# Kernel tuning notes

Hardware: AMD Instinct MI355X
Metric: run time of the kernel (lower is better)

Reference implementation:

```python
import jax, jax.numpy as jnp
import numpy as np

B, N, C = 2, 2048, 1024
H = 16
D = C // H  # head_dim = 64
SCALE = D ** -0.5


def setup_inputs() -> dict:
    key = jax.random.key(0)
    k1, k2, k3, k4 = jax.random.split(key, 4)
    x = jax.random.normal(k1, (B, N, C), dtype=jnp.float32)
    # nn.Linear(in_dim, 3*out_dim, bias=False): store as [in, 3*out] for x @ W
    w_qkv = jax.random.normal(k2, (C, 3 * C), dtype=jnp.float32) * (C ** -0.5)
    w_proj = jax.random.normal(k3, (C, C), dtype=jnp.float32) * (C ** -0.5)
    b_proj = jax.random.normal(k4, (C,), dtype=jnp.float32) * 0.01
    return {"x": x, "w_qkv": w_qkv, "w_proj": w_proj, "b_proj": b_proj}


def reference(x, w_qkv, w_proj, b_proj):
    b, n, c = x.shape
    # QKV projection -> [3, B, H, N, D]
    qkv = (x @ w_qkv).reshape(b, n, 3, H, D).transpose(2, 0, 3, 1, 4)
    q, k, v = qkv[0], qkv[1], qkv[2]
    # scaled dot-product attention, full [B, H, N, N] scores as in original
    attn = jax.nn.softmax(jnp.einsum('bhqd,bhkd->bhqk', q * SCALE, k), axis=-1)
    out = jnp.einsum('bhqk,bhkd->bhqd', attn, v)  # [B, H, N, D]
    out = out.transpose(0, 2, 1, 3).reshape(b, n, c)
    return out @ w_proj + b_proj
```

## Files before the change

### kernel.cpp

```cpp
#include <hip/hip_runtime.h>

typedef unsigned short u16;
typedef float f32x4 __attribute__((ext_vector_type(4)));
typedef short bf16x8 __attribute__((ext_vector_type(8)));
typedef u16 u16x4 __attribute__((ext_vector_type(4)));
typedef u16 u16x8 __attribute__((ext_vector_type(8)));
typedef __bf16 bfr4 __attribute__((ext_vector_type(4)));

#define BB 2
#define NN 2048
#define CC 1024
#define HH 16
#define DD 64
#define MM (BB * NN)
#define NQKV (3 * CC)
#define QSCALE 0.18033688011112042f

#if __has_builtin(__builtin_amdgcn_exp2f)
#define EXP2(x) __builtin_amdgcn_exp2f(x)
#else
#define EXP2(x) exp2f(x)
#endif

__device__ __forceinline__ u16 f2bf(float f) {
    unsigned u = __float_as_uint(f);
    u += 0x7FFFu + ((u >> 16) & 1u);
    return (u16)(u >> 16);
}

__device__ __forceinline__ void ld_lds16(const u16* g, u16* l) {
    __builtin_amdgcn_global_load_lds(
        (const __attribute__((address_space(1))) unsigned int*)g,
        (__attribute__((address_space(3))) unsigned int*)l, 16, 0, 0);
}

__global__ __launch_bounds__(256) void k_prep(const float* __restrict__ x,
                                              const float* __restrict__ wqkv,
                                              const float* __restrict__ wproj,
                                              u16* __restrict__ Xb,
                                              u16* __restrict__ Wq,
                                              u16* __restrict__ Wp) {
    __shared__ float tile[64][65];
    int bid = blockIdx.x, t = threadIdx.x;
    if (bid < 2048) {
        int i = (bid * 256 + t) * 8;
        float4 a = *(const float4*)(x + i);
        float4 b = *(const float4*)(x + i + 4);
        u16x8 o;
        o[0] = f2bf(a.x); o[1] = f2bf(a.y); o[2] = f2bf(a.z); o[3] = f2bf(a.w);
        o[4] = f2bf(b.x); o[5] = f2bf(b.y); o[6] = f2bf(b.z); o[7] = f2bf(b.w);
        *(u16x8*)(Xb + i) = o;
        return;
    }
    const float* in;
    u16* out;
    int Nn, n0, k0;
    if (bid < 2048 + 768) {
        int b2 = bid - 2048;
        in = wqkv; out = Wq; Nn = NQKV;
        n0 = (b2 % 48) * 64; k0 = (b2 / 48) * 64;
    } else {
        int b3 = bid - 2816;
        in = wproj; out = Wp; Nn = CC;
        n0 = (b3 & 15) * 64; k0 = (b3 >> 4) * 64;
    }
    int tx = t & 63, ty = t >> 6;
#pragma unroll
    for (int r = 0; r < 64; r += 4)
        tile[ty + r][tx] = in[(size_t)(k0 + ty + r) * Nn + n0 + tx];
    __syncthreads();
#pragma unroll
    for (int r = 0; r < 64; r += 4)
        out[(size_t)(n0 + ty + r) * CC + k0 + tx] = f2bf(tile[tx][ty + r]);
}

__global__ __launch_bounds__(512, 2) void k_gemmq(
    const u16* __restrict__ A, const u16* __restrict__ B,
    u16* __restrict__ Qb, u16* __restrict__ Kb, u16* __restrict__ Vb) {
    const int Kd = 1024;
    __shared__ __align__(16) u16 Ah0[256][64], Bh0[192][64];
    __shared__ __align__(16) u16 Ah1[256][64], Bh1[192][64];

    int t = threadIdx.x, wave = t >> 6, lane = t & 63;
    int quad = lane >> 4, l16 = lane & 15;
    int wr = wave >> 2, wc = wave & 3;

    int cid = blockIdx.y * 16 + blockIdx.x;
    int swz = (cid & 7) * 32 + (cid >> 3);
    int m0 = (swz >> 4) * 256, n0 = (swz & 15) * 192;

    int strow = wave * 8 + (lane >> 3);
    int stdst = (lane & 7) * 8;
    int stsrc = ((lane & 7) ^ (lane >> 3)) * 8;

    f32x4 acc[8][3];
#pragma unroll
    for (int i = 0; i < 8; i++)
#pragma unroll
        for (int j = 0; j < 3; j++) acc[i][j] = f32x4{0.f, 0.f, 0.f, 0.f};

    auto STAGE = [&](int k0, u16 (*Ad)[64], u16 (*Bd)[64]) {
#pragma unroll
        for (int i = 0; i < 4; i++) {
            int row = i * 64 + strow;
            ld_lds16(A + (size_t)(m0 + row) * Kd + k0 + stsrc, &Ad[row][stdst]);
        }
#pragma unroll
        for (int i = 0; i < 3; i++) {
            int row = i * 64 + strow;
            ld_lds16(B + (size_t)(n0 + row) * Kd + k0 + stsrc, &Bd[row][stdst]);
        }
    };
    auto COMPUTE = [&](u16 (*As)[64], u16 (*Bs)[64]) {
#pragma unroll
        for (int s = 0; s < 2; s++) {
            int pos = ((s * 4 + quad) ^ (l16 & 7)) * 8;
            bf16x8 af[8], bg[3];
#pragma unroll
            for (int m = 0; m < 8; m++)
                af[m] = *(const bf16x8*)&As[wr * 128 + m * 16 + l16][pos];
#pragma unroll
            for (int n = 0; n < 3; n++)
                bg[n] = *(const bf16x8*)&Bs[wc * 48 + n * 16 + l16][pos];
            __builtin_amdgcn_s_setprio(1);
#pragma unroll
            for (int m = 0; m < 8; m++)
#pragma unroll
                for (int n = 0; n < 3; n++)
                    acc[m][n] = __builtin_amdgcn_mfma_f32_16x16x32_bf16(
                        af[m], bg[n], acc[m][n], 0, 0, 0);
            __builtin_amdgcn_s_setprio(0);
        }
    };

    STAGE(0, Ah0, Bh0);
    __syncthreads();
    for (int k0 = 0; k0 < Kd; k0 += 128) {
        STAGE(k0 + 64, Ah1, Bh1);
        COMPUTE(Ah0, Bh0);
        __syncthreads();
        if (k0 + 128 < Kd) STAGE(k0 + 128, Ah0, Bh0);
        COMPUTE(Ah1, Bh1);
        __syncthreads();
    }

#pragma unroll
    for (int m = 0; m < 8; m++)
#pragma unroll
        for (int n = 0; n < 3; n++)
#pragma unroll
            for (int r = 0; r < 4; r++) {
                int grow = m0 + wr * 128 + m * 16 + quad * 4 + r;
                int gcol = n0 + wc * 48 + n * 16 + l16;
                float v = acc[m][n][r];
                int three = gcol >> 10, rem = gcol & 1023;
                int h = rem >> 6, d = rem & 63;
                int bb = grow >> 11, nn = grow & 2047;
                if (three == 0) {
                    Qb[((size_t)(bb * HH + h) * NN + nn) * DD + d] = f2bf(v * QSCALE);
                } else if (three == 1) {
                    Kb[((size_t)(bb * HH + h) * NN + nn) * DD + d] = f2bf(v);
                } else {
                    Vb[((size_t)(bb * HH + h) * DD + d) * NN + nn] = f2bf(v);
                }
            }
}

__global__ __launch_bounds__(256) void k_gemmp(
    const u16* __restrict__ A, const u16* __restrict__ B,
    const float* __restrict__ bias, float* __restrict__ Cout) {
    const int Kd = 1024;
    __shared__ __align__(16) u16 Ah[64][128];
    __shared__ __align__(16) u16 Bh[128][128];

    int t = threadIdx.x, wave = t >> 6, lane = t & 63;
    int quad = lane >> 4, l16 = lane & 15;
    int m0 = blockIdx.x * 64, n0 = blockIdx.y * 128;

    int strow = lane >> 4;
    int stdst = (lane & 15) * 8;

    f32x4 acc[4][2];
#pragma unroll
    for (int i = 0; i < 4; i++)
#pragma unroll
        for (int j = 0; j < 2; j++) acc[i][j] = f32x4{0.f, 0.f, 0.f, 0.f};

    auto STAGE = [&](int k0) {
#pragma unroll
        for (int i = 0; i < 4; i++) {
            int row = wave * 16 + i * 4 + strow;
            int src = ((lane & 15) ^ (row & 7)) * 8;
            ld_lds16(A + (size_t)(m0 + row) * Kd + k0 + src, &Ah[row & 63][0] + stdst);
        }
#pragma unroll
        for (int i = 0; i < 8; i++) {
            int row = wave * 32 + i * 4 + strow;
            int src = ((lane & 15) ^ (row & 7)) * 8;
            ld_lds16(B + (size_t)(n0 + row) * Kd + k0 + src, &Bh[row & 127][0] + stdst);
        }
    };
    auto COMPUTE = [&]() {
#pragma unroll
        for (int s = 0; s < 4; s++) {
            int pos = ((s * 4 + quad) ^ (l16 & 7)) * 8;
            bf16x8 af[4], bg[2];
#pragma unroll
            for (int m = 0; m < 4; m++)
                af[m] = *(const bf16x8*)&Ah[m * 16 + l16][pos];
#pragma unroll
            for (int n = 0; n < 2; n++)
                bg[n] = *(const bf16x8*)&Bh[wave * 32 + n * 16 + l16][pos];
            __builtin_amdgcn_s_setprio(1);
#pragma unroll
            for (int m = 0; m < 4; m++)
#pragma unroll
                for (int n = 0; n < 2; n++)
                    acc[m][n] = __builtin_amdgcn_mfma_f32_16x16x32_bf16(
                        af[m], bg[n], acc[m][n], 0, 0, 0);
            __builtin_amdgcn_s_setprio(0);
        }
    };

    for (int k0 = 0; k0 < Kd; k0 += 128) {
        __syncthreads();
        STAGE(k0);
        __syncthreads();
        COMPUTE();
    }

#pragma unroll
    for (int m = 0; m < 4; m++)
#pragma unroll
        for (int n = 0; n < 2; n++)
#pragma unroll
            for (int r = 0; r < 4; r++) {
                int grow = m0 + m * 16 + quad * 4 + r;
                int gcol = n0 + wave * 32 + n * 16 + l16;
                Cout[(size_t)grow * CC + gcol] = acc[m][n][r] + bias[gcol];
            }
}

__global__ __launch_bounds__(512) void k_attn(const u16* __restrict__ Qb,
                                              const u16* __restrict__ Kb,
                                              const u16* __restrict__ VbT,
                                              u16* __restrict__ Ob) {
    __shared__ __align__(16) u16 Ks0[64][64], Ks1[64][64];
    __shared__ __align__(16) u16 Vs0[64][64], Vs1[64][64];
    __shared__ __align__(16) u16 Ps[8][32][72];

    int t = threadIdx.x, wave = t >> 6, lane = t & 63;
    int quad = lane >> 4, l16 = lane & 15;
    int bh = blockIdx.x, q0 = blockIdx.y * 256;
    const size_t kbase = (size_t)bh * NN * DD;
    const size_t vbase = (size_t)bh * DD * NN;

    bf16x8 qf[2][2];
#pragma unroll
    for (int qj = 0; qj < 2; qj++) {
        int qrow = q0 + wave * 32 + qj * 16 + l16;
        qf[qj][0] = *(const bf16x8*)&Qb[kbase + (size_t)qrow * DD + quad * 8];
        qf[qj][1] = *(const bf16x8*)&Qb[kbase + (size_t)qrow * DD + 32 + quad * 8];
    }

    f32x4 o[2][4];
#pragma unroll
    for (int qj = 0; qj < 2; qj++)
#pragma unroll
        for (int i = 0; i < 4; i++) o[qj][i] = f32x4{0.f, 0.f, 0.f, 0.f};
    f32x4 lrow[2] = {f32x4{0.f, 0.f, 0.f, 0.f}, f32x4{0.f, 0.f, 0.f, 0.f}};

    int stgrp = lane & 7;
    int stsrc = (stgrp ^ (lane >> 3)) * 8;
    int strow = wave * 8 + (lane >> 3);
    int cf0 = (quad ^ (l16 & 7)) * 8;
    int cf1 = ((4 + quad) ^ (l16 & 7)) * 8;

    auto STAGE = [&](int cc, u16 (*Kd_)[64], u16 (*Vd_)[64]) {
        ld_lds16(&Kb[kbase + (size_t)(cc * 64 + strow) * DD + stsrc],
                 &Kd_[strow][stgrp * 8]);
        ld_lds16(&VbT[vbase + (size_t)strow * NN + cc * 64 + stsrc],
                 &Vd_[strow][stgrp * 8]);
    };

    auto COMPUTE = [&](u16 (*Ksrc)[64], u16 (*Vsrc)[64]) {
        bf16x8 kf[4][2];
#pragma unroll
        for (int kt = 0; kt < 4; kt++) {
            kf[kt][0] = *(const bf16x8*)&Ksrc[kt * 16 + l16][cf0];
            kf[kt][1] = *(const bf16x8*)&Ksrc[kt * 16 + l16][cf1];
        }
#pragma unroll
        for (int qj = 0; qj < 2; qj++) {
            f32x4 s[4];
            __builtin_amdgcn_s_setprio(1);
#pragma unroll
            for (int kt = 0; kt < 4; kt++) {
                f32x4 z = f32x4{0.f, 0.f, 0.f, 0.f};
                z = __builtin_amdgcn_mfma_f32_16x16x32_bf16(kf[kt][0], qf[qj][0], z, 0, 0, 0);
                z = __builtin_amdgcn_mfma_f32_16x16x32_bf16(kf[kt][1], qf[qj][1], z, 0, 0, 0);
                s[kt] = z;
            }
            __builtin_amdgcn_s_setprio(0);
#pragma unroll
            for (int kt = 0; kt < 4; kt++) {
                bfr4 pk;
#pragma unroll
                for (int r = 0; r < 4; r++) {
                    float e = EXP2(s[kt][r]);
                    lrow[qj][r] += e;
                    pk[r] = (__bf16)e;
                }
                *(bfr4*)&Ps[wave][qj * 16 + l16][kt * 16 + quad * 4] = pk;
            }
        }
        __asm__ volatile("s_waitcnt lgkmcnt(0)" ::: "memory");
        bf16x8 pb[2][2];
#pragma unroll
        for (int qj = 0; qj < 2; qj++) {
            pb[qj][0] = *(const bf16x8*)&Ps[wave][qj * 16 + l16][quad * 8];
            pb[qj][1] = *(const bf16x8*)&Ps[wave][qj * 16 + l16][32 + quad * 8];
        }
        __builtin_amdgcn_s_setprio(1);
#pragma unroll
        for (int dt = 0; dt < 4; dt++) {
            bf16x8 vf0 = *(const bf16x8*)&Vsrc[dt * 16 + l16][cf0];
            bf16x8 vf1 = *(const bf16x8*)&Vsrc[dt * 16 + l16][cf1];
#pragma unroll
            for (int qj = 0; qj < 2; qj++) {
                o[qj][dt] = __builtin_amdgcn_mfma_f32_16x16x32_bf16(vf0, pb[qj][0], o[qj][dt], 0, 0, 0);
                o[qj][dt] = __builtin_amdgcn_mfma_f32_16x16x32_bf16(vf1, pb[qj][1], o[qj][dt], 0, 0, 0);
            }
        }
        __builtin_amdgcn_s_setprio(0);
    };

    STAGE(0, Ks0, Vs0);
    __syncthreads();

    for (int c = 0; c < NN / 64; c += 2) {
        STAGE(c + 1, Ks1, Vs1);
        COMPUTE(Ks0, Vs0);
        __syncthreads();
        if (c + 2 < NN / 64) STAGE(c + 2, Ks0, Vs0);
        COMPUTE(Ks1, Vs1);
        __syncthreads();
    }

    int b = bh >> 4, h = bh & 15;
#pragma unroll
    for (int qj = 0; qj < 2; qj++) {
        float l = (lrow[qj][0] + lrow[qj][1]) + (lrow[qj][2] + lrow[qj][3]);
        l += __shfl_xor(l, 16, 64);
        l += __shfl_xor(l, 32, 64);
        float inv = 1.f / l;
        int grow = b * NN + q0 + wave * 32 + qj * 16 + l16;
#pragma unroll
        for (int dt = 0; dt < 4; dt++) {
            u16x4 hv;
#pragma unroll
            for (int r = 0; r < 4; r++) hv[r] = f2bf(o[qj][dt][r] * inv);
            int gcol = h * DD + dt * 16 + quad * 4;
            *(u16x4*)&Ob[(size_t)grow * CC + gcol] = hv;
        }
    }
}

extern "C" void kernel_launch(void* const* d_in, const int* in_sizes, int n_in,
                              void* d_out, int out_size, void* d_ws, size_t ws_size,
                              hipStream_t stream) {
    const float* x      = (const float*)d_in[0];
    const float* w_qkv  = (const float*)d_in[1];
    const float* w_proj = (const float*)d_in[2];
    const float* b_proj = (const float*)d_in[3];
    float* out = (float*)d_out;

    u16* p = (u16*)d_ws;
    u16* Xb = p; p += (size_t)MM * CC;
    u16* Wq = p; p += (size_t)NQKV * CC;
    u16* Wp = p; p += (size_t)CC * CC;
    u16* Qb = p; p += (size_t)MM * CC;
    u16* Kb = p; p += (size_t)MM * CC;
    u16* Vb = p; p += (size_t)MM * CC;
    u16* Ob = p; p += (size_t)MM * CC;

    k_prep<<<2048 + 768 + 256, 256, 0, stream>>>(x, w_qkv, w_proj, Xb, Wq, Wp);
    k_gemmq<<<dim3(NQKV / 192, MM / 256), 512, 0, stream>>>(Xb, Wq, Qb, Kb, Vb);
    k_attn<<<dim3(BB * HH, NN / 256), 512, 0, stream>>>(Qb, Kb, Vb, Ob);
    k_gemmp<<<dim3(MM / 64, CC / 128), 256, 0, stream>>>(Ob, Wp, b_proj, out);
}
```

Before: 184.8 us.

## Double-buffer projection GEMM with larger 128x128 tiles and 512 threads

The output-projection GEMM now uses 128x128 block tiles with 8 waves in a 2x4 layout, instead of 64x128 with 4 waves. It also double-buffers LDS so the next K tile's async loads overlap the MFMA compute on the current tile, and it halves the number of barriers per tile. The intent is to hide global-load latency and improve reuse. The cost is 128KB of LDS per block and half as many blocks in the grid, which may reduce occupancy and device fill.

New measurement: 180.5 us. 2.3% less time.

```diff
diff --git a/kernel.cpp b/kernel.cpp
--- a/kernel.cpp
+++ b/kernel.cpp
@@ -166,18 +166,19 @@
             }
 }
 
-__global__ __launch_bounds__(256) void k_gemmp(
+__global__ __launch_bounds__(512, 2) void k_gemmp(
     const u16* __restrict__ A, const u16* __restrict__ B,
     const float* __restrict__ bias, float* __restrict__ Cout) {
     const int Kd = 1024;
-    __shared__ __align__(16) u16 Ah[64][128];
-    __shared__ __align__(16) u16 Bh[128][128];
+    __shared__ __align__(16) u16 Ah0[128][128], Bh0[128][128];
+    __shared__ __align__(16) u16 Ah1[128][128], Bh1[128][128];
 
     int t = threadIdx.x, wave = t >> 6, lane = t & 63;
     int quad = lane >> 4, l16 = lane & 15;
-    int m0 = blockIdx.x * 64, n0 = blockIdx.y * 128;
-
-    int strow = lane >> 4;
+    int wr = wave >> 2, wc = wave & 3;
+    int m0 = blockIdx.x * 128, n0 = blockIdx.y * 128;
+
+    int strow = wave * 4 + (lane >> 4);
     int stdst = (lane & 15) * 8;
 
     f32x4 acc[4][2];
@@ -186,31 +187,31 @@
 #pragma unroll
         for (int j = 0; j < 2; j++) acc[i][j] = f32x4{0.f, 0.f, 0.f, 0.f};
 
-    auto STAGE = [&](int k0) {
+    auto STAGE = [&](int k0, u16 (*Ad)[128], u16 (*Bd)[128]) {
 #pragma unroll
         for (int i = 0; i < 4; i++) {
-            int row = wave * 16 + i * 4 + strow;
+            int row = i * 32 + strow;
             int src = ((lane & 15) ^ (row & 7)) * 8;
-            ld_lds16(A + (size_t)(m0 + row) * Kd + k0 + src, &Ah[row & 63][0] + stdst);
-        }
-#pragma unroll
-        for (int i = 0; i < 8; i++) {
-            int row = wave * 32 + i * 4 + strow;
+            ld_lds16(A + (size_t)(m0 + row) * Kd + k0 + src, &Ad[row][stdst]);
+        }
+#pragma unroll
+        for (int i = 0; i < 4; i++) {
+            int row = i * 32 + strow;
             int src = ((lane & 15) ^ (row & 7)) * 8;
-            ld_lds16(B + (size_t)(n0 + row) * Kd + k0 + src, &Bh[row & 127][0] + stdst);
-        }
-    };
-    auto COMPUTE = [&]() {
+            ld_lds16(B + (size_t)(n0 + row) * Kd + k0 + src, &Bd[row][stdst]);
+        }
+    };
+    auto COMPUTE = [&](u16 (*As)[128], u16 (*Bs)[128]) {
 #pragma unroll
         for (int s = 0; s < 4; s++) {
             int pos = ((s * 4 + quad) ^ (l16 & 7)) * 8;
             bf16x8 af[4], bg[2];
 #pragma unroll
             for (int m = 0; m < 4; m++)
-                af[m] = *(const bf16x8*)&Ah[m * 16 + l16][pos];
+                af[m] = *(const bf16x8*)&As[wr * 64 + m * 16 + l16][pos];
 #pragma unroll
             for (int n = 0; n < 2; n++)
-                bg[n] = *(const bf16x8*)&Bh[wave * 32 + n * 16 + l16][pos];
+                bg[n] = *(const bf16x8*)&Bs[wc * 32 + n * 16 + l16][pos];
             __builtin_amdgcn_s_setprio(1);
 #pragma unroll
             for (int m = 0; m < 4; m++)
@@ -222,11 +223,15 @@
         }
     };
 
-    for (int k0 = 0; k0 < Kd; k0 += 128) {
-        __syncthreads();
-        STAGE(k0);
-        __syncthreads();
-        COMPUTE();
+    STAGE(0, Ah0, Bh0);
+    __syncthreads();
+    for (int k0 = 0; k0 < Kd; k0 += 256) {
+        STAGE(k0 + 128, Ah1, Bh1);
+        COMPUTE(Ah0, Bh0);
+        __syncthreads();
+        if (k0 + 256 < Kd) STAGE(k0 + 256, Ah0, Bh0);
+        COMPUTE(Ah1, Bh1);
+        __syncthreads();
     }
 
 #pragma unroll
@@ -235,8 +240,8 @@
         for (int n = 0; n < 2; n++)
 #pragma unroll
             for (int r = 0; r < 4; r++) {
-                int grow = m0 + m * 16 + quad * 4 + r;
-                int gcol = n0 + wave * 32 + n * 16 + l16;
+                int grow = m0 + wr * 64 + m * 16 + quad * 4 + r;
+                int gcol = n0 + wc * 32 + n * 16 + l16;
                 Cout[(size_t)grow * CC + gcol] = acc[m][n][r] + bias[gcol];
             }
 }
@@ -387,5 +392,5 @@
     k_prep<<<2048 + 768 + 256, 256, 0, stream>>>(x, w_qkv, w_proj, Xb, Wq, Wp);
     k_gemmq<<<dim3(NQKV / 192, MM / 256), 512, 0, stream>>>(Xb, Wq, Qb, Kb, Vb);
     k_attn<<<dim3(BB * HH, NN / 256), 512, 0, stream>>>(Qb, Kb, Vb, Ob);
-    k_gemmp<<<dim3(MM / 64, CC / 128), 256, 0, stream>>>(Ob, Wp, b_proj, out);
-}
+    k_gemmp<<<dim3(MM / 128, CC / 128), 512, 0, stream>>>(Ob, Wp, b_proj, out);
+}
```
